# Optimization experiments

Measured on AMD Instinct MI355X. Metric: run time of the kernel, lower is better.

The kernel has to match this reference:

```python
import jax, jax.numpy as jnp
import numpy as np

ALPHA = 0.25
GAMMA = 2.0
EPS = 1e-8
W_CLASS = 2.0
W_BBOX = 5.0
W_GIOU = 2.0
PROB_THRESH = 0.5
BBOX_THRESH = -0.1
BIG = 1e9  # cost assigned to filtered-out (masked) pseudo targets


def box_cxcywh_to_xyxy(b):
    cx, cy, w, h = b[..., 0], b[..., 1], b[..., 2], b[..., 3]
    return jnp.stack([cx - 0.5 * w, cy - 0.5 * h, cx + 0.5 * w, cy + 0.5 * h], axis=-1)


def generalized_box_iou(boxes1, boxes2):
    # boxes1: [..., N, 4] xyxy, boxes2: [..., M, 4] xyxy -> [..., N, M]
    area1 = (boxes1[..., 2] - boxes1[..., 0]) * (boxes1[..., 3] - boxes1[..., 1])
    area2 = (boxes2[..., 2] - boxes2[..., 0]) * (boxes2[..., 3] - boxes2[..., 1])
    lt = jnp.maximum(boxes1[..., :, None, :2], boxes2[..., None, :, :2])
    rb = jnp.minimum(boxes1[..., :, None, 2:], boxes2[..., None, :, 2:])
    wh = jnp.clip(rb - lt, 0.0)
    inter = wh[..., 0] * wh[..., 1]
    union = area1[..., :, None] + area2[..., None, :] - inter
    iou = inter / union
    lt_c = jnp.minimum(boxes1[..., :, None, :2], boxes2[..., None, :, :2])
    rb_c = jnp.maximum(boxes1[..., :, None, 2:], boxes2[..., None, :, 2:])
    wh_c = jnp.clip(rb_c - lt_c, 0.0)
    area_c = wh_c[..., 0] * wh_c[..., 1]
    return iou - (area_c - union) / area_c


def setup_inputs() -> dict:
    key = jax.random.key(0)
    k1, k2, k3, k4, k5 = jax.random.split(key, 5)
    B, Q, C, T = 32, 900, 91, 30
    return {
        "pred_logits": jax.random.normal(k1, (B, Q, C), dtype=jnp.float32),
        "pred_boxes": jax.random.uniform(k2, (B, Q, 4), dtype=jnp.float32),
        "pred_logits_base": jax.random.normal(k3, (B, Q, C), dtype=jnp.float32),
        "pred_boxes_base": jax.random.uniform(k4, (B, Q, 4), dtype=jnp.float32),
        "targets_boxes": jax.random.uniform(k5, (B, T, 4), dtype=jnp.float32),
    }


def reference(pred_logits, pred_boxes, pred_logits_base, pred_boxes_base, targets_boxes):
    # ---- pseudo-label generation from the base model (original: sort + python filter) ----
    prob_base = jax.nn.sigmoid(pred_logits_base)          # [B, Qb, C]
    top_prob = jnp.max(prob_base, axis=-1)                # [B, Qb]
    pseudo_labels = jnp.argmax(prob_base, axis=-1)        # [B, Qb] (idx_base[..., 0])
    keep_prob = top_prob > PROB_THRESH
    # original per-box loop: keep if all(-giou(pseudo, gt) > bbox_thresh)
    g_pt = generalized_box_iou(box_cxcywh_to_xyxy(pred_boxes_base),
                               box_cxcywh_to_xyxy(targets_boxes))  # [B, Qb, T]
    keep_giou = jnp.all(-g_pt > BBOX_THRESH, axis=-1)     # [B, Qb]
    pseudo_mask = keep_prob & keep_giou                   # valid pseudo-target slots

    # ---- cost matrix between current predictions and pseudo targets ----
    out_prob = jax.nn.sigmoid(pred_logits)                # [B, Q, C]
    # gather class prob at each pseudo target's label: [B, Q, Qb]
    p = jnp.take_along_axis(out_prob, pseudo_labels[:, None, :], axis=2)
    pos_cost = ALPHA * (1.0 - p) ** GAMMA * (-jnp.log(p + EPS))
    neg_cost = (1.0 - ALPHA) * p ** GAMMA * (-jnp.log(1.0 - p + EPS))
    cost_class = pos_cost - neg_cost

    # L1 cdist between cxcywh boxes: [B, Q, Qb]
    cost_bbox = jnp.sum(jnp.abs(pred_boxes[:, :, None, :] - pred_boxes_base[:, None, :, :]), axis=-1)

    cost_giou = -generalized_box_iou(box_cxcywh_to_xyxy(pred_boxes),
                                     box_cxcywh_to_xyxy(pred_boxes_base))  # [B, Q, Qb]

    C = W_BBOX * cost_bbox + W_CLASS * cost_class + W_GIOU * cost_giou
    # masked (filtered-out) pseudo targets get a huge cost so they are never matched
    C = jnp.where(pseudo_mask[:, None, :], C, BIG)
    return C, pseudo_mask
```

## Files before the change

kernel.cpp:

```cpp
#include <hip/hip_runtime.h>

typedef float f32x4 __attribute__((ext_vector_type(4)));

static constexpr int B  = 32;
static constexpr int Q  = 900;
static constexpr int NC = 91;
static constexpr int T  = 30;
static constexpr int QT = 12;

static constexpr float ALPHA_ = 0.25f;
static constexpr float EPS_   = 1e-8f;
static constexpr float BIG_   = 1e9f;

static constexpr int K1_BLOCKS = (B * Q) / 4;
static constexpr int N4        = B * Q * NC / 4;
static constexpr int K2_BLOCKS = (N4 + 255) / 256;

__device__ __forceinline__ float class_cost(float x) {
  float p   = __builtin_amdgcn_rcpf(1.0f + __expf(-x));
  float omp = 1.0f - p;
  float pos = ALPHA_ * (omp * omp) * (-__logf(p + EPS_));
  float neg = (1.0f - ALPHA_) * (p * p) * (-__logf(omp + EPS_));
  return pos - neg;
}

__device__ void mask_label_body(int wid, int lane,
                                const float* __restrict__ logits_base,
                                const float4* __restrict__ boxes_base,
                                const float4* __restrict__ targets,
                                int* __restrict__ labels,
                                float* __restrict__ mask_out) {
#pragma clang fp contract(off)
  int b = wid / Q;

  const float* row = logits_base + (size_t)wid * NC;
  float v  = (lane < NC) ? row[lane] : -1e30f;
  int  arg = lane;
  int lane2 = lane + 64;
  if (lane2 < NC) {
    float v2 = row[lane2];
    if (v2 > v) { v = v2; arg = lane2; }
  }
  for (int off = 32; off >= 1; off >>= 1) {
    float ov = __shfl_xor(v, off, 64);
    int   oi = __shfl_xor(arg, off, 64);
    if (ov > v || (ov == v && oi < arg)) { v = ov; arg = oi; }
  }
  bool keep = (v > 0.0f);

  float4 bb = boxes_base[wid];
  float x1 = bb.x - 0.5f * bb.z, y1 = bb.y - 0.5f * bb.w;
  float x2 = bb.x + 0.5f * bb.z, y2 = bb.y + 0.5f * bb.w;
  float a1 = (x2 - x1) * (y2 - y1);

  bool ok = true;
  if (lane < T) {
    float4 tb = targets[b * T + lane];
    float tx1 = tb.x - 0.5f * tb.z, ty1 = tb.y - 0.5f * tb.w;
    float tx2 = tb.x + 0.5f * tb.z, ty2 = tb.y + 0.5f * tb.w;
    float a2 = (tx2 - tx1) * (ty2 - ty1);
    float ltx = fmaxf(x1, tx1), lty = fmaxf(y1, ty1);
    float rbx = fminf(x2, tx2), rby = fminf(y2, ty2);
    float iw = fmaxf(rbx - ltx, 0.0f), ih = fmaxf(rby - lty, 0.0f);
    float inter = iw * ih;
    float uni = (a1 + a2) - inter;
    float iou = inter / uni;
    float cx1 = fminf(x1, tx1), cy1 = fminf(y1, ty1);
    float cx2 = fmaxf(x2, tx2), cy2 = fmaxf(y2, ty2);
    float cw = fmaxf(cx2 - cx1, 0.0f), ch = fmaxf(cy2 - cy1, 0.0f);
    float ac = cw * ch;
    float g = iou - (ac - uni) / ac;
    ok = (-g > -0.1f);
  }
  keep = keep && __all(ok);

  if (lane == 0) {
    labels[wid]   = arg;
    mask_out[wid] = keep ? 1.0f : 0.0f;
  }
}

__global__ __launch_bounds__(256) void k12(
    const float* __restrict__ logits_base,
    const float4* __restrict__ boxes_base,
    const float4* __restrict__ targets,
    int* __restrict__ labels,
    float* __restrict__ mask_out,
    const f32x4* __restrict__ lg4,
    f32x4* __restrict__ cc4) {
  int tid = threadIdx.x;
  if (blockIdx.x < K1_BLOCKS) {
    int wid = (blockIdx.x * 256 + tid) >> 6;
    mask_label_body(wid, tid & 63, logits_base, boxes_base, targets,
                    labels, mask_out);
  } else {
    int i = (blockIdx.x - K1_BLOCKS) * 256 + tid;
    if (i < N4) {
      f32x4 v = __builtin_nontemporal_load(lg4 + i);
      f32x4 o;
      o.x = class_cost(v.x);
      o.y = class_cost(v.y);
      o.z = class_cost(v.z);
      o.w = class_cost(v.w);
      cc4[i] = o;
    }
  }
}

__global__ __launch_bounds__(256, 4) void k3_cost(
    const float* __restrict__ cc_all,
    const float4* __restrict__ pred_boxes,
    const float4* __restrict__ boxes_base,
    const int* __restrict__ labels,
    const float* __restrict__ mask_in,
    float* __restrict__ Cout) {
  __shared__ float  s_cc[QT * NC];
  __shared__ float4 s_e[QT];
  __shared__ float4 s_m[QT];
  __shared__ float  s_pa[QT];

  int b   = blockIdx.x / (Q / QT);
  int q0  = (blockIdx.x % (Q / QT)) * QT;
  int tid = threadIdx.x;

  const f32x4* ccs = reinterpret_cast<const f32x4*>(
      cc_all + ((size_t)(b * Q + q0)) * NC);
  f32x4* sc4 = reinterpret_cast<f32x4*>(s_cc);
  for (int i = tid; i < QT * NC / 4; i += 256)
    sc4[i] = __builtin_nontemporal_load(ccs + i);

  if (tid < QT) {
    float4 pb = pred_boxes[b * Q + q0 + tid];
    float px1 = pb.x - 0.5f * pb.z, py1 = pb.y - 0.5f * pb.w;
    float px2 = pb.x + 0.5f * pb.z, py2 = pb.y + 0.5f * pb.w;
    s_e[tid]  = make_float4(px1, py1, px2, py2);
    s_m[tid]  = make_float4(px1 + px2, py1 + py2, pb.z, pb.w);
    s_pa[tid] = (px2 - px1) * (py2 - py1);
  }

  bool active = (tid < Q / 4);
  float x1b[4], y1b[4], x2b[4], y2b[4], wb[4], hb[4], c2big[4];
  const float* pk[4];
  int jbase = b * Q + 4 * tid;
  if (active) {
    int4 lbv = *reinterpret_cast<const int4*>(labels + jbase);
    float4 mkv = *reinterpret_cast<const float4*>(mask_in + jbase);
    pk[0] = s_cc + lbv.x; pk[1] = s_cc + lbv.y;
    pk[2] = s_cc + lbv.z; pk[3] = s_cc + lbv.w;
    c2big[0] = 2.0f + (mkv.x != 0.0f ? 0.0f : BIG_);
    c2big[1] = 2.0f + (mkv.y != 0.0f ? 0.0f : BIG_);
    c2big[2] = 2.0f + (mkv.z != 0.0f ? 0.0f : BIG_);
    c2big[3] = 2.0f + (mkv.w != 0.0f ? 0.0f : BIG_);
#pragma unroll
    for (int k = 0; k < 4; ++k) {
      float4 bb = boxes_base[jbase + k];
      x1b[k] = bb.x - 0.5f * bb.z; y1b[k] = bb.y - 0.5f * bb.w;
      x2b[k] = bb.x + 0.5f * bb.z; y2b[k] = bb.y + 0.5f * bb.w;
      wb[k]  = bb.z; hb[k] = bb.w;
    }
  }
  __syncthreads();

  if (active) {
    size_t rowbase = ((size_t)(b * Q + q0)) * Q + 4 * tid;
#pragma unroll
    for (int qi = 0; qi < QT; ++qi, rowbase += Q) {
      float4 pe = s_e[qi];
      float4 pm = s_m[qi];
      float  pa = s_pa[qi];
      float res[4];
#pragma unroll
      for (int k = 0; k < 4; ++k) {
        float cls = pk[k][qi * NC];
        float dx = pm.x - (x1b[k] + x2b[k]);
        float dy = pm.y - (y1b[k] + y2b[k]);
        float dw = pm.z - wb[k];
        float dh = pm.w - hb[k];
        float l1 = fmaf(0.5f, fabsf(dx) + fabsf(dy), fabsf(dw) + fabsf(dh));
        float mwx = fminf(pe.z, x2b[k]) - fmaxf(pe.x, x1b[k]);
        float mwy = fminf(pe.w, y2b[k]) - fmaxf(pe.y, y1b[k]);
        float inter = fmaxf(mwx, 0.0f) * fmaxf(mwy, 0.0f);
        float uni = fmaf(wb[k], hb[k], pa) - inter;
        float cw = (pm.z + wb[k]) - mwx;
        float ch = (pm.w + hb[k]) - mwy;
        float acl = cw * ch;
        float r = __builtin_amdgcn_rcpf(uni * acl);
        float t = fmaf(inter, acl, uni * uni) * r;
        res[k] = fmaf(-2.0f, t, fmaf(5.0f, l1, fmaf(2.0f, cls, c2big[k])));
      }
      f32x4 out4 = {res[0], res[1], res[2], res[3]};
      __builtin_nontemporal_store(out4,
          reinterpret_cast<f32x4*>(Cout + rowbase));
    }
  }
}

extern "C" void kernel_launch(void* const* d_in, const int* in_sizes, int n_in,
                              void* d_out, int out_size, void* d_ws, size_t ws_size,
                              hipStream_t stream) {
  const float*  pred_logits      = (const float*)d_in[0];
  const float4* pred_boxes       = (const float4*)d_in[1];
  const float*  pred_logits_base = (const float*)d_in[2];
  const float4* pred_boxes_base  = (const float4*)d_in[3];
  const float4* targets          = (const float4*)d_in[4];

  float* out      = (float*)d_out;
  float* mask_out = out + (size_t)B * Q * Q;

  int*   labels = (int*)d_ws;
  float* cc     = (float*)((char*)d_ws + 131072);

  k12<<<K1_BLOCKS + K2_BLOCKS, 256, 0, stream>>>(
      pred_logits_base, pred_boxes_base, targets, labels, mask_out,
      (const f32x4*)pred_logits, (f32x4*)cc);

  k3_cost<<<B * (Q / QT), 256, 0, stream>>>(
      cc, pred_boxes, pred_boxes_base, labels, mask_out, out);
}
```

Before: 47.43 us.

## Fuse class-cost computation into cost kernel and drop intermediate buffer

The focal class-cost transform of pred_logits moves out of the first kernel and into the cost kernel. Each cost block now loads its 12 rows of raw logits, applies the transform, and writes the result straight into shared memory. This removes a full B*Q*NC intermediate write and read through global memory. The output store also changes from a nontemporal store to a plain float4 store, and the first kernel becomes a mask/label-only kernel with fewer blocks. In exchange the cost kernel does more transcendental work per block before its barrier.

```diff
diff --git a/kernel.cpp b/kernel.cpp
--- a/kernel.cpp
+++ b/kernel.cpp
@@ -12,25 +12,15 @@
 static constexpr float EPS_   = 1e-8f;
 static constexpr float BIG_   = 1e9f;
 
-static constexpr int K1_BLOCKS = (B * Q) / 4;
-static constexpr int N4        = B * Q * NC / 4;
-static constexpr int K2_BLOCKS = (N4 + 255) / 256;
-
-__device__ __forceinline__ float class_cost(float x) {
-  float p   = __builtin_amdgcn_rcpf(1.0f + __expf(-x));
-  float omp = 1.0f - p;
-  float pos = ALPHA_ * (omp * omp) * (-__logf(p + EPS_));
-  float neg = (1.0f - ALPHA_) * (p * p) * (-__logf(omp + EPS_));
-  return pos - neg;
-}
-
-__device__ void mask_label_body(int wid, int lane,
-                                const float* __restrict__ logits_base,
-                                const float4* __restrict__ boxes_base,
-                                const float4* __restrict__ targets,
-                                int* __restrict__ labels,
-                                float* __restrict__ mask_out) {
+__global__ __launch_bounds__(256) void k1_mask_label(
+    const float* __restrict__ logits_base,
+    const float4* __restrict__ boxes_base,
+    const float4* __restrict__ targets,
+    int* __restrict__ labels,
+    float* __restrict__ mask_out) {
 #pragma clang fp contract(off)
+  int wid  = (blockIdx.x * 256 + threadIdx.x) >> 6;
+  int lane = threadIdx.x & 63;
   int b = wid / Q;
 
   const float* row = logits_base + (size_t)wid * NC;
@@ -80,35 +70,16 @@
   }
 }
 
-__global__ __launch_bounds__(256) void k12(
-    const float* __restrict__ logits_base,
-    const float4* __restrict__ boxes_base,
-    const float4* __restrict__ targets,
-    int* __restrict__ labels,
-    float* __restrict__ mask_out,
-    const f32x4* __restrict__ lg4,
-    f32x4* __restrict__ cc4) {
-  int tid = threadIdx.x;
-  if (blockIdx.x < K1_BLOCKS) {
-    int wid = (blockIdx.x * 256 + tid) >> 6;
-    mask_label_body(wid, tid & 63, logits_base, boxes_base, targets,
-                    labels, mask_out);
-  } else {
-    int i = (blockIdx.x - K1_BLOCKS) * 256 + tid;
-    if (i < N4) {
-      f32x4 v = __builtin_nontemporal_load(lg4 + i);
-      f32x4 o;
-      o.x = class_cost(v.x);
-      o.y = class_cost(v.y);
-      o.z = class_cost(v.z);
-      o.w = class_cost(v.w);
-      cc4[i] = o;
-    }
-  }
+__device__ __forceinline__ float class_cost(float x) {
+  float p   = __builtin_amdgcn_rcpf(1.0f + __expf(-x));
+  float omp = 1.0f - p;
+  float pos = ALPHA_ * (omp * omp) * (-__logf(p + EPS_));
+  float neg = (1.0f - ALPHA_) * (p * p) * (-__logf(omp + EPS_));
+  return pos - neg;
 }
 
 __global__ __launch_bounds__(256, 4) void k3_cost(
-    const float* __restrict__ cc_all,
+    const float* __restrict__ pred_logits,
     const float4* __restrict__ pred_boxes,
     const float4* __restrict__ boxes_base,
     const int* __restrict__ labels,
@@ -123,11 +94,18 @@
   int q0  = (blockIdx.x % (Q / QT)) * QT;
   int tid = threadIdx.x;
 
-  const f32x4* ccs = reinterpret_cast<const f32x4*>(
-      cc_all + ((size_t)(b * Q + q0)) * NC);
+  const f32x4* lg4 = reinterpret_cast<const f32x4*>(
+      pred_logits + ((size_t)(b * Q + q0)) * NC);
   f32x4* sc4 = reinterpret_cast<f32x4*>(s_cc);
-  for (int i = tid; i < QT * NC / 4; i += 256)
-    sc4[i] = __builtin_nontemporal_load(ccs + i);
+  for (int i = tid; i < QT * NC / 4; i += 256) {
+    f32x4 v = __builtin_nontemporal_load(lg4 + i);
+    f32x4 o;
+    o.x = class_cost(v.x);
+    o.y = class_cost(v.y);
+    o.z = class_cost(v.z);
+    o.w = class_cost(v.w);
+    sc4[i] = o;
+  }
 
   if (tid < QT) {
     float4 pb = pred_boxes[b * Q + q0 + tid];
@@ -188,9 +166,8 @@
         float t = fmaf(inter, acl, uni * uni) * r;
         res[k] = fmaf(-2.0f, t, fmaf(5.0f, l1, fmaf(2.0f, cls, c2big[k])));
       }
-      f32x4 out4 = {res[0], res[1], res[2], res[3]};
-      __builtin_nontemporal_store(out4,
-          reinterpret_cast<f32x4*>(Cout + rowbase));
+      *reinterpret_cast<float4*>(Cout + rowbase) =
+          make_float4(res[0], res[1], res[2], res[3]);
     }
   }
 }
@@ -207,13 +184,11 @@
   float* out      = (float*)d_out;
   float* mask_out = out + (size_t)B * Q * Q;
 
-  int*   labels = (int*)d_ws;
-  float* cc     = (float*)((char*)d_ws + 131072);
+  int* labels = (int*)d_ws;
 
-  k12<<<K1_BLOCKS + K2_BLOCKS, 256, 0, stream>>>(
-      pred_logits_base, pred_boxes_base, targets, labels, mask_out,
-      (const f32x4*)pred_logits, (f32x4*)cc);
+  k1_mask_label<<<(B * Q) / 4, 256, 0, stream>>>(
+      pred_logits_base, pred_boxes_base, targets, labels, mask_out);
 
   k3_cost<<<B * (Q / QT), 256, 0, stream>>>(
-      cc, pred_boxes, pred_boxes_base, labels, mask_out, out);
+      pred_logits, pred_boxes, pred_boxes_base, labels, mask_out, out);
 }
```

New measurement: 48.24 us. About the same (+1.7%).
